# Kernel optimization log

Measured on AMD Instinct MI355X. Metric: run time of the kernel, lower is better.

Reference implementation:

```python
import jax, jax.numpy as jnp
import numpy as np

B, S, D = 2, 4096, 256
H, KD = 8, 256  # keras MHA built with key_dim=d_model -> per-head dim = 256
DFF = 1024
EPS = 1e-3  # keras LayerNormalization default epsilon
NEG = 1e9


def setup_inputs() -> dict:
    key = jax.random.key(0)
    ks = jax.random.split(key, 16)
    sd = 0.02
    return {
        "x": jax.random.normal(ks[0], (B, S, D), jnp.float32),
        "w_2": 128,
        "Wq": jax.random.normal(ks[1], (D, H, KD), jnp.float32) * sd,
        "bq": jnp.zeros((H, KD), jnp.float32),
        "Wk": jax.random.normal(ks[2], (D, H, KD), jnp.float32) * sd,
        "bk": jnp.zeros((H, KD), jnp.float32),
        "Wv": jax.random.normal(ks[3], (D, H, KD), jnp.float32) * sd,
        "bv": jnp.zeros((H, KD), jnp.float32),
        "Wo": jax.random.normal(ks[4], (H, KD, D), jnp.float32) * sd,
        "bo": jnp.zeros((D,), jnp.float32),
        "W1": jax.random.normal(ks[5], (D, DFF), jnp.float32) * sd,
        "b1": jnp.zeros((DFF,), jnp.float32),
        "W2": jax.random.normal(ks[6], (DFF, D), jnp.float32) * sd,
        "b2": jnp.zeros((D,), jnp.float32),
        "g1": jnp.ones((D,), jnp.float32),
        "be1": jnp.zeros((D,), jnp.float32),
        "g2": jnp.ones((D,), jnp.float32),
        "be2": jnp.zeros((D,), jnp.float32),
    }


def layer_norm(x, g, b):
    mu = jnp.mean(x, axis=-1, keepdims=True)
    var = jnp.mean(jnp.square(x - mu), axis=-1, keepdims=True)
    return (x - mu) * jax.lax.rsqrt(var + EPS) * g + b


def reference(x, w_2, Wq, bq, Wk, bk, Wv, bv, Wo, bo, W1, b1, W2, b2, g1, be1, g2, be2):
    # --- sliding-window self attention (dense scores + mask, as in source) ---
    q = jnp.einsum('bsd,dhk->bshk', x, Wq) + bq
    k = jnp.einsum('bsd,dhk->bshk', x, Wk) + bk
    v = jnp.einsum('bsd,dhk->bshk', x, Wv) + bv
    scores = jnp.einsum('bqhd,bkhd->bhqk', q, k) / jnp.sqrt(jnp.asarray(KD, x.dtype))
    idx = jnp.arange(S)
    mask = (jnp.abs(idx[:, None] - idx[None, :]) <= w_2)  # [S, S]
    scores = scores + (1.0 - mask.astype(x.dtype)) * (-NEG)
    attn = jax.nn.softmax(scores, axis=-1)
    ctx = jnp.einsum('bhqk,bkhd->bqhd', attn, v)
    attn_out = jnp.einsum('bqhd,hdo->bqo', ctx, Wo) + bo
    x = layer_norm(x + attn_out, g1, be1)
    # --- feed-forward ---
    h = jax.nn.relu(jnp.einsum('bsd,df->bsf', x, W1) + b1)
    ffn = jnp.einsum('bsf,fd->bsd', h, W2) + b2
    x = layer_norm(x + ffn, g2, be2)
    return x
```

## Files before the change

### kernel.cpp

```cpp
#include <hip/hip_runtime.h>
#include <hip/hip_bf16.h>

#define Bn 2
#define Sn 4096
#define Dn 256
#define Hn 8
#define KDn 256
#define DFFn 1024
#define Mn (Bn*Sn)
#define NQKVn (Hn*KDn)

typedef __attribute__((ext_vector_type(4))) float f32x4;
typedef __attribute__((ext_vector_type(8))) short bf16x8;
typedef __attribute__((ext_vector_type(4))) short short4v;

__device__ __forceinline__ short f2bf(float f) {
  unsigned u = __builtin_bit_cast(unsigned, f);
  unsigned r = u + 0x7fffu + ((u >> 16) & 1u);
  return (short)(r >> 16);
}

#define GLL16(gsrc, ldst) \
  __builtin_amdgcn_global_load_lds((const __attribute__((address_space(1))) void*)(gsrc), \
                                   (__attribute__((address_space(3))) void*)(ldst), 16, 0, 0)

#define WAITCNT4 asm volatile("s_waitcnt vmcnt(4)" ::: "memory")
#define WAITCNT2 asm volatile("s_waitcnt vmcnt(2)" ::: "memory")
#define WAITCNT0 asm volatile("s_waitcnt vmcnt(0)" ::: "memory")
#define BARRIER  do { __builtin_amdgcn_s_barrier(); asm volatile("" ::: "memory"); } while (0)

__global__ __launch_bounds__(256)
void cvt_x(const float* __restrict__ x, short* __restrict__ xb, int n) {
  int i = (blockIdx.x * 256 + threadIdx.x) * 4;
  if (i < n) {
    float4 v = *(const float4*)(x + i);
    short4v o = { f2bf(v.x), f2bf(v.y), f2bf(v.z), f2bf(v.w) };
    *(short4v*)(xb + i) = o;
  }
}

__global__ __launch_bounds__(256)
void concat_bias(const float* __restrict__ bq, const float* __restrict__ bk,
                 const float* __restrict__ bv, float* __restrict__ o) {
  int i = blockIdx.x * 256 + threadIdx.x;
  o[i] = (i < 2048) ? bq[i] : (i < 4096 ? bk[i - 2048] : bv[i - 4096]);
}

__global__ __launch_bounds__(256)
void cvt_weights(const float* __restrict__ Wq, const float* __restrict__ Wk,
                 const float* __restrict__ Wv, const float* __restrict__ Wo,
                 const float* __restrict__ W1, const float* __restrict__ W2,
                 short* __restrict__ WqT, short* __restrict__ WkT,
                 short* __restrict__ WvT, short* __restrict__ WoT,
                 short* __restrict__ W1T, short* __restrict__ W2T) {
  int t = blockIdx.x;
  const float* W; short* WT; int K, N;
  if      (t < 512)  { W = Wq; WT = WqT; K = 256;  N = 2048; }
  else if (t < 1024) { t -= 512;  W = Wk; WT = WkT; K = 256;  N = 2048; }
  else if (t < 1536) { t -= 1024; W = Wv; WT = WvT; K = 256;  N = 2048; }
  else if (t < 2048) { t -= 1536; W = Wo; WT = WoT; K = 2048; N = 256;  }
  else if (t < 2304) { t -= 2048; W = W1; WT = W1T; K = 256;  N = 1024; }
  else               { t -= 2304; W = W2; WT = W2T; K = 1024; N = 256;  }
  const int ktiles = K >> 5;
  const int k0 = (t % ktiles) * 32, n0 = (t / ktiles) * 32;
  __shared__ short tt[32][33];
  const int tx = threadIdx.x & 31, ty = threadIdx.x >> 5;
#pragma unroll
  for (int i = 0; i < 32; i += 8)
    tt[ty + i][tx] = f2bf(W[(size_t)(k0 + ty + i) * N + n0 + tx]);
  __syncthreads();
#pragma unroll
  for (int i = 0; i < 32; i += 8)
    WT[(size_t)(n0 + ty + i) * K + k0 + tx] = tt[tx][ty + i];
}

__global__ __launch_bounds__(256, 3)
void gemm_qkv(const short* __restrict__ A, const short* __restrict__ BT,
              const float* __restrict__ bias, short* __restrict__ Qo,
              short* __restrict__ Ko, short* __restrict__ Vto) {
  __shared__ __align__(16) short smem[3 * 8192];
  const int tid = threadIdx.x;
  const int lane = tid & 63;
  const int wave = tid >> 6;
  const int tn = blockIdx.x;
  const int tm = blockIdx.y;
  const int wr = (wave >> 1) * 64;
  const int wc = (wave & 1) * 64;
  const int lrow = lane & 15;
  const int lk = (lane >> 4) * 8;

  f32x4 acc[4][4];
#pragma unroll
  for (int i = 0; i < 4; ++i)
#pragma unroll
    for (int j = 0; j < 4; ++j) acc[i][j] = (f32x4){0.f, 0.f, 0.f, 0.f};

  const int row_s = tid >> 2;
  const int col_s = (tid & 3) * 8;
  const short* aB = A + (size_t)(tm * 128 + row_s) * 256 + col_s;
  const short* bB = BT + (size_t)(tn * 128 + row_s) * 256 + col_s;

  auto stage = [&](int kt, int bf) {
    const short* aP = aB + kt * 32;
    const short* bP = bB + kt * 32;
    short* AsB = smem + bf * 8192 + wave * 512;
    short* BsB = smem + bf * 8192 + 4096 + wave * 512;
    GLL16(aP, AsB);
    GLL16(aP + 64 * 256, AsB + 2048);
    GLL16(bP, BsB);
    GLL16(bP + 64 * 256, BsB + 2048);
  };

  stage(0, 0);
  stage(1, 1);
  int cur = 0;
  for (int kt = 0; kt < 8; ++kt) {
    if (kt == 7) WAITCNT0; else WAITCNT4;
    BARRIER;
    if (kt + 2 < 8) { int nb = cur + 2; if (nb >= 3) nb -= 3; stage(kt + 2, nb); }
    const short* As = smem + cur * 8192;
    const short* Bs = As + 4096;
    bf16x8 af[4], bfr[4];
#pragma unroll
    for (int i = 0; i < 4; ++i) {
      af[i]  = *(const bf16x8*)(As + (wr + i * 16 + lrow) * 32 + lk);
      bfr[i] = *(const bf16x8*)(Bs + (wc + i * 16 + lrow) * 32 + lk);
    }
#pragma unroll
    for (int i = 0; i < 4; ++i)
#pragma unroll
      for (int j = 0; j < 4; ++j)
        acc[i][j] = __builtin_amdgcn_mfma_f32_16x16x32_bf16(af[i], bfr[j], acc[i][j], 0, 0, 0);
    ++cur; if (cur == 3) cur = 0;
  }

  const int rbase = (lane >> 4) * 4;
  if (tn < 32) {
    short* C = (tn < 16) ? Qo : Ko;
    const float sc = (tn < 16) ? 1.f : 0.0625f;
    const int cb = (tn & 15) * 128;
#pragma unroll
    for (int j = 0; j < 4; ++j) {
      const int cj = wc + j * 16 + lrow;
      const float bv = bias[tn * 128 + cj];
      const int cl = cb + cj;
#pragma unroll
      for (int i = 0; i < 4; ++i) {
        const int row0 = tm * 128 + wr + i * 16 + rbase;
        f32x4 a = acc[i][j];
#pragma unroll
        for (int r = 0; r < 4; ++r)
          C[(size_t)(row0 + r) * NQKVn + cl] = f2bf((a[r] + bv) * sc);
      }
    }
  } else {
    __syncthreads();
    short* Ct = smem;
#pragma unroll
    for (int j = 0; j < 4; ++j) {
      const int colL = wc + j * 16 + lrow;
      const float bv = bias[tn * 128 + colL];
#pragma unroll
      for (int i = 0; i < 4; ++i) {
        const int rowL0 = wr + i * 16 + rbase;
        f32x4 a = acc[i][j];
        short4v o = { f2bf(a[0] + bv), f2bf(a[1] + bv), f2bf(a[2] + bv), f2bf(a[3] + bv) };
        *(short4v*)(&Ct[colL * 130 + rowL0]) = o;
      }
    }
    __syncthreads();
    const int kd_l = tid >> 1;
    const int so = (tid & 1) * 64;
    const int cl = (tn - 32) * 128 + kd_l;
    const int hh = cl >> 8;
    const int kd = cl & 255;
    const int row0 = tm * 128;
    const int bb = row0 >> 12;
    const int s0 = (row0 & (Sn - 1)) + so;
    short* dst = Vto + (size_t)((bb * Hn + hh) * KDn + kd) * Sn + s0;
#pragma unroll
    for (int u = 0; u < 64; u += 8)
      *(bf16x8*)(dst + u) = *(const bf16x8*)(&Ct[kd_l * 130 + so + u]);
  }
}

__global__ __launch_bounds__(256, 3)
void gemm_ffn1(const short* __restrict__ A, const short* __restrict__ BT,
               const float* __restrict__ bias, short* __restrict__ C,
               int N, int K) {
  __shared__ __align__(16) short smem[3 * 8192];
  const int tid = threadIdx.x;
  const int lane = tid & 63;
  const int wave = tid >> 6;
  const int tn = blockIdx.x;
  const int tm = blockIdx.y;
  const int wr = (wave >> 1) * 64;
  const int wc = (wave & 1) * 64;
  const int lrow = lane & 15;
  const int lk = (lane >> 4) * 8;

  f32x4 acc[4][4];
#pragma unroll
  for (int i = 0; i < 4; ++i)
#pragma unroll
    for (int j = 0; j < 4; ++j) acc[i][j] = (f32x4){0.f, 0.f, 0.f, 0.f};

  const int row_s = tid >> 2;
  const int col_s = (tid & 3) * 8;
  const short* aB = A + (size_t)(tm * 128 + row_s) * K + col_s;
  const short* bB = BT + (size_t)(tn * 128 + row_s) * K + col_s;

  auto stage = [&](int kt, int bf) {
    const short* aP = aB + kt * 32;
    const short* bP = bB + kt * 32;
    short* AsB = smem + bf * 8192 + wave * 512;
    short* BsB = smem + bf * 8192 + 4096 + wave * 512;
    GLL16(aP, AsB);
    GLL16(aP + (size_t)64 * K, AsB + 2048);
    GLL16(bP, BsB);
    GLL16(bP + (size_t)64 * K, BsB + 2048);
  };

  const int nk = K >> 5;
  stage(0, 0);
  if (nk > 1) stage(1, 1);
  int cur = 0;
  for (int kt = 0; kt < nk; ++kt) {
    if (kt == nk - 1) WAITCNT0; else WAITCNT4;
    BARRIER;
    if (kt + 2 < nk) { int nb = cur + 2; if (nb >= 3) nb -= 3; stage(kt + 2, nb); }
    const short* As = smem + cur * 8192;
    const short* Bs = As + 4096;
    bf16x8 af[4], bfr[4];
#pragma unroll
    for (int i = 0; i < 4; ++i) {
      af[i]  = *(const bf16x8*)(As + (wr + i * 16 + lrow) * 32 + lk);
      bfr[i] = *(const bf16x8*)(Bs + (wc + i * 16 + lrow) * 32 + lk);
    }
#pragma unroll
    for (int i = 0; i < 4; ++i)
#pragma unroll
      for (int j = 0; j < 4; ++j)
        acc[i][j] = __builtin_amdgcn_mfma_f32_16x16x32_bf16(af[i], bfr[j], acc[i][j], 0, 0, 0);
    ++cur; if (cur == 3) cur = 0;
  }

  const int rbase = (lane >> 4) * 4;
#pragma unroll
  for (int j = 0; j < 4; ++j) {
    const int col = tn * 128 + wc + j * 16 + lrow;
    const float bv = bias[col];
#pragma unroll
    for (int i = 0; i < 4; ++i) {
      const int row0 = tm * 128 + wr + i * 16 + rbase;
      f32x4 a = acc[i][j];
#pragma unroll
      for (int r = 0; r < 4; ++r)
        C[(size_t)(row0 + r) * N + col] = f2bf(fmaxf(a[r] + bv, 0.f));
    }
  }
}

__global__ __launch_bounds__(256, 4)
void gemm_bt64(const short* __restrict__ A, const short* __restrict__ BT,
               const float* __restrict__ bias, float* __restrict__ C,
               int N, int K) {
  __shared__ __align__(16) short smem[3 * 4096];
  const int tid = threadIdx.x;
  const int lane = tid & 63;
  const int wave = tid >> 6;
  const int tn = blockIdx.x;
  const int tm = blockIdx.y;
  const int wr = (wave >> 1) * 32;
  const int wc = (wave & 1) * 32;
  const int lrow = lane & 15;
  const int lk = (lane >> 4) * 8;

  f32x4 acc[2][2];
#pragma unroll
  for (int i = 0; i < 2; ++i)
#pragma unroll
    for (int j = 0; j < 2; ++j) acc[i][j] = (f32x4){0.f, 0.f, 0.f, 0.f};

  const int row_s = tid >> 2;
  const int col_s = (tid & 3) * 8;
  const short* aB = A + (size_t)(tm * 64 + row_s) * K + col_s;
  const short* bB = BT + (size_t)(tn * 64 + row_s) * K + col_s;

  auto stage = [&](int kt, int bf) {
    GLL16(aB + kt * 32, smem + bf * 4096 + wave * 512);
    GLL16(bB + kt * 32, smem + bf * 4096 + 2048 + wave * 512);
  };

  const int nk = K >> 5;
  stage(0, 0);
  if (nk > 1) stage(1, 1);
  int cur = 0;
  for (int kt = 0; kt < nk; ++kt) {
    if (kt == nk - 1) WAITCNT0; else WAITCNT2;
    BARRIER;
    if (kt + 2 < nk) { int nb = cur + 2; if (nb >= 3) nb -= 3; stage(kt + 2, nb); }
    const short* As = smem + cur * 4096;
    const short* Bs = As + 2048;
    bf16x8 af[2], bfr[2];
#pragma unroll
    for (int i = 0; i < 2; ++i) {
      af[i]  = *(const bf16x8*)(As + (wr + i * 16 + lrow) * 32 + lk);
      bfr[i] = *(const bf16x8*)(Bs + (wc + i * 16 + lrow) * 32 + lk);
    }
#pragma unroll
    for (int i = 0; i < 2; ++i)
#pragma unroll
      for (int j = 0; j < 2; ++j)
        acc[i][j] = __builtin_amdgcn_mfma_f32_16x16x32_bf16(af[i], bfr[j], acc[i][j], 0, 0, 0);
    ++cur; if (cur == 3) cur = 0;
  }

  const int rbase = (lane >> 4) * 4;
#pragma unroll
  for (int j = 0; j < 2; ++j) {
    const int col = tn * 64 + wc + j * 16 + lrow;
    const float bv = bias[col];
#pragma unroll
    for (int i = 0; i < 2; ++i) {
      const int row0 = tm * 64 + wr + i * 16 + rbase;
      f32x4 a = acc[i][j];
#pragma unroll
      for (int r = 0; r < 4; ++r) C[(size_t)(row0 + r) * N + col] = a[r] + bv;
    }
  }
}

__global__ __launch_bounds__(512, 1)
void attn_win(const short* __restrict__ q, const short* __restrict__ k,
              const short* __restrict__ vt, short* __restrict__ ctx,
              const int* __restrict__ w2p) {
  const int bid = blockIdx.x;
  const int swz = (bid & 7) * 32 + (bid >> 3);
  const int q0 = (swz & 15) * 256;
  const int h = (swz >> 4) & 7;
  const int b = swz >> 7;
  const int tid = threadIdx.x;
  const int lane = tid & 63;
  const int wave = tid >> 6;
  const int w2 = *w2p;
  const int qw = q0 + wave * 32;
  const int lrow = lane & 15;
  const int lk = (lane >> 4) * 8;
  const int lk2 = lk * 2;
  const int rbase = (lane >> 4) * 4;

  __shared__ __align__(16) short Ks[3][8192];
  __shared__ __align__(16) short Vs[3][8192];
  __shared__ __align__(16) short Ps[8][1024];
  short* P = Ps[wave];

  const short* qbase = q + (size_t)(b * Sn + qw) * NQKVn + h * KDn;
  bf16x8 qf[2][8];
#pragma unroll
  for (int mi = 0; mi < 2; ++mi)
#pragma unroll
    for (int ks = 0; ks < 8; ++ks)
      qf[mi][ks] = *(const bf16x8*)(qbase + (size_t)(mi * 16 + lrow) * NQKVn + ks * 32 + lk);

  f32x4 oacc[2][16];
#pragma unroll
  for (int mi = 0; mi < 2; ++mi)
#pragma unroll
    for (int nc = 0; nc < 16; ++nc) oacc[mi][nc] = (f32x4){0.f, 0.f, 0.f, 0.f};

  float lsum[2][4];
#pragma unroll
  for (int mi = 0; mi < 2; ++mi)
#pragma unroll
    for (int r = 0; r < 4; ++r) lsum[mi][r] = 0.f;

  const short* kbase = k + (size_t)(b * Sn) * NQKVn + h * KDn;
  const short* vtb = vt + (size_t)((b * Hn + h) * KDn) * Sn;

  int bstart = q0 - w2; if (bstart < 0) bstart = 0; bstart &= ~31;
  int bend = q0 + 256 + w2; if (bend > Sn) bend = Sn; bend = (bend + 31) & ~31;
  int wlo = qw - w2; if (wlo < 0) wlo = 0; wlo &= ~31;
  int whi = qw + 32 + w2; if (whi > Sn) whi = Sn;

  auto stage = [&](int c0, int bf) {
#pragma unroll
    for (int e = 0; e < 2; ++e) {
      const int o = e * 8192 + tid * 16;
      const int row = o >> 9;
      const int cc = (o & 511) ^ ((row & 7) << 4);
      GLL16(kbase + (size_t)(c0 + row) * NQKVn + (cc >> 1),
            (char*)Ks[bf] + e * 8192 + wave * 1024);
    }
#pragma unroll
    for (int e = 0; e < 2; ++e) {
      const int o = e * 8192 + tid * 16;
      const int row = o >> 6;
      const int cc = (o & 63) ^ ((row & 3) << 4);
      GLL16(vtb + (size_t)row * Sn + c0 + (cc >> 1),
            (char*)Vs[bf] + e * 8192 + wave * 1024);
    }
  };

  const int nch = (bend - bstart) >> 5;
  stage(bstart, 0);
  if (nch > 1) stage(bstart + 32, 1);

  int cur = 0;
  for (int i = 0; i < nch; ++i) {
    const int c0 = bstart + i * 32;
    if (i == nch - 1) WAITCNT0; else WAITCNT4;
    BARRIER;
    if (i + 2 < nch) { int nb = cur + 2; if (nb >= 3) nb -= 3; stage(c0 + 64, nb); }

    if (c0 >= wlo && c0 < whi) {
      const char* Kc = (const char*)Ks[cur];
      const int x0 = (lrow & 7) << 4;
      f32x4 sf[2][2];
      sf[0][0] = sf[0][1] = sf[1][0] = sf[1][1] = (f32x4){0.f, 0.f, 0.f, 0.f};
#pragma unroll
      for (int ks = 0; ks < 8; ++ks) {
        const int cb = (lk2 + ks * 64) ^ x0;
        bf16x8 kf0 = *(const bf16x8*)(Kc + lrow * 512 + cb);
        bf16x8 kf1 = *(const bf16x8*)(Kc + (16 + lrow) * 512 + cb);
        sf[0][0] = __builtin_amdgcn_mfma_f32_16x16x32_bf16(qf[0][ks], kf0, sf[0][0], 0, 0, 0);
        sf[0][1] = __builtin_amdgcn_mfma_f32_16x16x32_bf16(qf[0][ks], kf1, sf[0][1], 0, 0, 0);
        sf[1][0] = __builtin_amdgcn_mfma_f32_16x16x32_bf16(qf[1][ks], kf0, sf[1][0], 0, 0, 0);
        sf[1][1] = __builtin_amdgcn_mfma_f32_16x16x32_bf16(qf[1][ks], kf1, sf[1][1], 0, 0, 0);
      }
      const bool full = (c0 >= qw + 31 - w2) && (c0 + 31 <= qw + w2);
      if (full) {
#pragma unroll
        for (int mi = 0; mi < 2; ++mi)
#pragma unroll
          for (int ni = 0; ni < 2; ++ni)
#pragma unroll
            for (int r = 0; r < 4; ++r) {
              const float p = __expf(sf[mi][ni][r]);
              sf[mi][ni][r] = p;
              lsum[mi][r] += p;
            }
      } else {
#pragma unroll
        for (int mi = 0; mi < 2; ++mi)
#pragma unroll
          for (int ni = 0; ni < 2; ++ni) {
            const int kk = c0 + ni * 16 + lrow;
#pragma unroll
            for (int r = 0; r < 4; ++r) {
              const int dd = (qw + mi * 16 + rbase + r) - kk;
              const bool val = (dd <= w2) && (dd >= -w2);
              float p = __expf(sf[mi][ni][r]);
              p = val ? p : 0.f;
              sf[mi][ni][r] = p;
              lsum[mi][r] += p;
            }
          }
      }
#pragma unroll
      for (int mi = 0; mi < 2; ++mi)
#pragma unroll
        for (int ni = 0; ni < 2; ++ni)
#pragma unroll
          for (int r = 0; r < 4; ++r)
            P[(mi * 16 + rbase + r) * 32 + ni * 16 + lrow] = f2bf(sf[mi][ni][r]);

      bf16x8 pa0 = *(const bf16x8*)(P + lrow * 32 + lk);
      bf16x8 pa1 = *(const bf16x8*)(P + (16 + lrow) * 32 + lk);
      const char* Vc = (const char*)Vs[cur] + lrow * 64 + (lk2 ^ ((lrow & 3) << 4));
#pragma unroll
      for (int nc = 0; nc < 16; ++nc) {
        bf16x8 vf = *(const bf16x8*)(Vc + nc * 1024);
        oacc[0][nc] = __builtin_amdgcn_mfma_f32_16x16x32_bf16(pa0, vf, oacc[0][nc], 0, 0, 0);
        oacc[1][nc] = __builtin_amdgcn_mfma_f32_16x16x32_bf16(pa1, vf, oacc[1][nc], 0, 0, 0);
      }
    }
    ++cur; if (cur == 3) cur = 0;
  }

#pragma unroll
  for (int mi = 0; mi < 2; ++mi)
#pragma unroll
    for (int r = 0; r < 4; ++r) {
      float s = lsum[mi][r];
#pragma unroll
      for (int d = 1; d < 16; d <<= 1) s += __shfl_xor(s, d);
      lsum[mi][r] = 1.f / s;
    }

  short* cbase = ctx + (size_t)(b * Sn + qw) * NQKVn + h * KDn;
#pragma unroll
  for (int mi = 0; mi < 2; ++mi)
#pragma unroll
    for (int nc = 0; nc < 16; ++nc)
#pragma unroll
      for (int r = 0; r < 4; ++r)
        cbase[(size_t)(mi * 16 + rbase + r) * NQKVn + nc * 16 + lrow] =
            f2bf(oacc[mi][nc][r] * lsum[mi][r]);
}

__global__ __launch_bounds__(256)
void ln_fused(const float* __restrict__ xin, const float* __restrict__ yin,
              const float* __restrict__ g, const float* __restrict__ bb,
              float* __restrict__ of32, short* __restrict__ obf) {
  const int row = blockIdx.x * 4 + (threadIdx.x >> 6);
  const int lane = threadIdx.x & 63;
  const size_t base = (size_t)row * Dn + lane * 4;
  float4 a = *(const float4*)(xin + base);
  float4 bv = *(const float4*)(yin + base);
  float4 v = { a.x + bv.x, a.y + bv.y, a.z + bv.z, a.w + bv.w };
  float sum = v.x + v.y + v.z + v.w;
  float ssq = v.x * v.x + v.y * v.y + v.z * v.z + v.w * v.w;
#pragma unroll
  for (int d = 1; d < 64; d <<= 1) { sum += __shfl_xor(sum, d); ssq += __shfl_xor(ssq, d); }
  const float mu = sum * (1.f / Dn);
  const float var = ssq * (1.f / Dn) - mu * mu;
  const float rs = rsqrtf(var + 1e-3f);
  float4 gg = *(const float4*)(g + lane * 4);
  float4 bbv = *(const float4*)(bb + lane * 4);
  float4 o = { (v.x - mu) * rs * gg.x + bbv.x, (v.y - mu) * rs * gg.y + bbv.y,
               (v.z - mu) * rs * gg.z + bbv.z, (v.w - mu) * rs * gg.w + bbv.w };
  if (of32) *(float4*)(of32 + base) = o;
  if (obf) {
    short4v ob = { f2bf(o.x), f2bf(o.y), f2bf(o.z), f2bf(o.w) };
    *(short4v*)(obf + base) = ob;
  }
}

extern "C" void kernel_launch(void* const* d_in, const int* in_sizes, int n_in,
                              void* d_out, int out_size, void* d_ws, size_t ws_size,
                              hipStream_t stream) {
  const float* x   = (const float*)d_in[0];
  const int*   w2p = (const int*)d_in[1];
  const float* Wq  = (const float*)d_in[2];
  const float* bq  = (const float*)d_in[3];
  const float* Wk  = (const float*)d_in[4];
  const float* bk  = (const float*)d_in[5];
  const float* Wv  = (const float*)d_in[6];
  const float* bv  = (const float*)d_in[7];
  const float* Wo  = (const float*)d_in[8];
  const float* bo  = (const float*)d_in[9];
  const float* W1  = (const float*)d_in[10];
  const float* b1  = (const float*)d_in[11];
  const float* W2  = (const float*)d_in[12];
  const float* b2  = (const float*)d_in[13];
  const float* g1  = (const float*)d_in[14];
  const float* be1 = (const float*)d_in[15];
  const float* g2  = (const float*)d_in[16];
  const float* be2 = (const float*)d_in[17];
  float* out = (float*)d_out;

  char* ws = (char*)d_ws;
  size_t off = 0;
  auto alloc = [&](size_t bytes) { void* p = ws + off; off += (bytes + 255) & ~(size_t)255; return p; };
  short* xb    = (short*)alloc((size_t)Mn * Dn * 2);
  short* WqkvT = (short*)alloc((size_t)3 * NQKVn * Dn * 2);
  float* bqkv  = (float*)alloc((size_t)3 * NQKVn * 4);
  short* WoT   = (short*)alloc((size_t)Dn * NQKVn * 2);
  short* W1T   = (short*)alloc((size_t)DFFn * Dn * 2);
  short* W2T   = (short*)alloc((size_t)Dn * DFFn * 2);
  short* qb    = (short*)alloc((size_t)Mn * NQKVn * 2);
  short* kb    = (short*)alloc((size_t)Mn * NQKVn * 2);
  short* vtb   = (short*)alloc((size_t)Mn * NQKVn * 2);
  float* attn_out = (float*)alloc((size_t)Mn * Dn * 4);
  float* x1    = (float*)alloc((size_t)Mn * Dn * 4);
  short* ctxb = qb;
  short* x1b  = xb;
  short* hb   = kb;
  float* ffn  = attn_out;

  cvt_x<<<dim3(Mn * Dn / 1024), dim3(256), 0, stream>>>(x, xb, Mn * Dn);
  cvt_weights<<<dim3(2560), dim3(256), 0, stream>>>(
      Wq, Wk, Wv, Wo, W1, W2,
      WqkvT, WqkvT + (size_t)NQKVn * Dn, WqkvT + (size_t)2 * NQKVn * Dn,
      WoT, W1T, W2T);
  concat_bias<<<dim3(24), dim3(256), 0, stream>>>(bq, bk, bv, bqkv);

  gemm_qkv<<<dim3(48, 64), dim3(256), 0, stream>>>(xb, WqkvT, bqkv, qb, kb, vtb);

  attn_win<<<dim3(256), dim3(512), 0, stream>>>(qb, kb, vtb, ctxb, w2p);

  gemm_bt64<<<dim3(Dn / 64, Mn / 64), dim3(256), 0, stream>>>(ctxb, WoT, bo, attn_out, Dn, NQKVn);
  ln_fused<<<dim3(Mn / 4), dim3(256), 0, stream>>>(x, attn_out, g1, be1, x1, x1b);
  gemm_ffn1<<<dim3(DFFn / 128, Mn / 128), dim3(256), 0, stream>>>(x1b, W1T, b1, hb, DFFn, Dn);
  gemm_bt64<<<dim3(Dn / 64, Mn / 64), dim3(256), 0, stream>>>(hb, W2T, b2, ffn, Dn, DFFn);
  ln_fused<<<dim3(Mn / 4), dim3(256), 0, stream>>>(x1, ffn, g2, be2, out, (short*)nullptr);
}
```

Measured before the change: 187.5 us.

## Stage GEMM epilogues through LDS, add MFMA priority, use exp2 softmax, pad P

The Q/K and ReLU GEMM epilogues now write bf16 results into a padded LDS tile and then emit coalesced 16-byte row stores, replacing scattered 2-byte global stores. s_setprio is raised around the MFMA blocks in all GEMMs. The K scale folds in log2(e) so the attention kernel can use exp2f instead of __expf. The per-wave P buffer gets a row stride of 40 to reduce LDS bank conflicts. The cost is extra barriers and LDS traffic in the epilogues and slightly more shared memory in attention.

Result: slower. 201.9 us (+7.7%).

```diff
diff --git a/kernel.cpp b/kernel.cpp
--- a/kernel.cpp
+++ b/kernel.cpp
@@ -126,33 +126,43 @@
       af[i]  = *(const bf16x8*)(As + (wr + i * 16 + lrow) * 32 + lk);
       bfr[i] = *(const bf16x8*)(Bs + (wc + i * 16 + lrow) * 32 + lk);
     }
+    __builtin_amdgcn_s_setprio(1);
 #pragma unroll
     for (int i = 0; i < 4; ++i)
 #pragma unroll
       for (int j = 0; j < 4; ++j)
         acc[i][j] = __builtin_amdgcn_mfma_f32_16x16x32_bf16(af[i], bfr[j], acc[i][j], 0, 0, 0);
+    __builtin_amdgcn_s_setprio(0);
     ++cur; if (cur == 3) cur = 0;
   }
 
   const int rbase = (lane >> 4) * 4;
   if (tn < 32) {
     short* C = (tn < 16) ? Qo : Ko;
-    const float sc = (tn < 16) ? 1.f : 0.0625f;
+    const float sc = (tn < 16) ? 1.f : (0.0625f * 1.4426950408889634f);
     const int cb = (tn & 15) * 128;
+    __syncthreads();
+    short* Ct = smem;
 #pragma unroll
     for (int j = 0; j < 4; ++j) {
-      const int cj = wc + j * 16 + lrow;
-      const float bv = bias[tn * 128 + cj];
-      const int cl = cb + cj;
+      const int colL = wc + j * 16 + lrow;
+      const float bv = bias[tn * 128 + colL];
 #pragma unroll
       for (int i = 0; i < 4; ++i) {
-        const int row0 = tm * 128 + wr + i * 16 + rbase;
+        const int rowL = wr + i * 16 + rbase;
         f32x4 a = acc[i][j];
 #pragma unroll
         for (int r = 0; r < 4; ++r)
-          C[(size_t)(row0 + r) * NQKVn + cl] = f2bf((a[r] + bv) * sc);
+          Ct[(rowL + r) * 136 + colL] = f2bf((a[r] + bv) * sc);
       }
     }
+    __syncthreads();
+    const int row = tid >> 1;
+    const int seg = (tid & 1) * 64;
+    short* dst = C + (size_t)(tm * 128 + row) * NQKVn + cb + seg;
+#pragma unroll
+    for (int u = 0; u < 64; u += 8)
+      *(bf16x8*)(dst + u) = *(const bf16x8*)(&Ct[row * 136 + seg + u]);
   } else {
     __syncthreads();
     short* Ct = smem;
@@ -237,28 +247,39 @@
       af[i]  = *(const bf16x8*)(As + (wr + i * 16 + lrow) * 32 + lk);
       bfr[i] = *(const bf16x8*)(Bs + (wc + i * 16 + lrow) * 32 + lk);
     }
+    __builtin_amdgcn_s_setprio(1);
 #pragma unroll
     for (int i = 0; i < 4; ++i)
 #pragma unroll
       for (int j = 0; j < 4; ++j)
         acc[i][j] = __builtin_amdgcn_mfma_f32_16x16x32_bf16(af[i], bfr[j], acc[i][j], 0, 0, 0);
+    __builtin_amdgcn_s_setprio(0);
     ++cur; if (cur == 3) cur = 0;
   }
 
   const int rbase = (lane >> 4) * 4;
+  __syncthreads();
+  short* Ct = smem;
 #pragma unroll
   for (int j = 0; j < 4; ++j) {
-    const int col = tn * 128 + wc + j * 16 + lrow;
-    const float bv = bias[col];
+    const int colL = wc + j * 16 + lrow;
+    const float bv = bias[tn * 128 + colL];
 #pragma unroll
     for (int i = 0; i < 4; ++i) {
-      const int row0 = tm * 128 + wr + i * 16 + rbase;
+      const int rowL = wr + i * 16 + rbase;
       f32x4 a = acc[i][j];
 #pragma unroll
       for (int r = 0; r < 4; ++r)
-        C[(size_t)(row0 + r) * N + col] = f2bf(fmaxf(a[r] + bv, 0.f));
-    }
-  }
+        Ct[(rowL + r) * 136 + colL] = f2bf(fmaxf(a[r] + bv, 0.f));
+    }
+  }
+  __syncthreads();
+  const int row = tid >> 1;
+  const int seg = (tid & 1) * 64;
+  short* dst = C + (size_t)(tm * 128 + row) * N + tn * 128 + seg;
+#pragma unroll
+  for (int u = 0; u < 64; u += 8)
+    *(bf16x8*)(dst + u) = *(const bf16x8*)(&Ct[row * 136 + seg + u]);
 }
 
 __global__ __launch_bounds__(256, 4)
@@ -308,11 +329,13 @@
       af[i]  = *(const bf16x8*)(As + (wr + i * 16 + lrow) * 32 + lk);
       bfr[i] = *(const bf16x8*)(Bs + (wc + i * 16 + lrow) * 32 + lk);
     }
+    __builtin_amdgcn_s_setprio(1);
 #pragma unroll
     for (int i = 0; i < 2; ++i)
 #pragma unroll
       for (int j = 0; j < 2; ++j)
         acc[i][j] = __builtin_amdgcn_mfma_f32_16x16x32_bf16(af[i], bfr[j], acc[i][j], 0, 0, 0);
+    __builtin_amdgcn_s_setprio(0);
     ++cur; if (cur == 3) cur = 0;
   }
 
@@ -352,7 +375,7 @@
 
   __shared__ __align__(16) short Ks[3][8192];
   __shared__ __align__(16) short Vs[3][8192];
-  __shared__ __align__(16) short Ps[8][1024];
+  __shared__ __align__(16) short Ps[8][1280];
   short* P = Ps[wave];
 
   const short* qbase = q + (size_t)(b * Sn + qw) * NQKVn + h * KDn;
@@ -436,7 +459,7 @@
           for (int ni = 0; ni < 2; ++ni)
 #pragma unroll
             for (int r = 0; r < 4; ++r) {
-              const float p = __expf(sf[mi][ni][r]);
+              const float p = exp2f(sf[mi][ni][r]);
               sf[mi][ni][r] = p;
               lsum[mi][r] += p;
             }
@@ -450,7 +473,7 @@
             for (int r = 0; r < 4; ++r) {
               const int dd = (qw + mi * 16 + rbase + r) - kk;
               const bool val = (dd <= w2) && (dd >= -w2);
-              float p = __expf(sf[mi][ni][r]);
+              float p = exp2f(sf[mi][ni][r]);
               p = val ? p : 0.f;
               sf[mi][ni][r] = p;
               lsum[mi][r] += p;
@@ -463,10 +486,10 @@
         for (int ni = 0; ni < 2; ++ni)
 #pragma unroll
           for (int r = 0; r < 4; ++r)
-            P[(mi * 16 + rbase + r) * 32 + ni * 16 + lrow] = f2bf(sf[mi][ni][r]);
-
-      bf16x8 pa0 = *(const bf16x8*)(P + lrow * 32 + lk);
-      bf16x8 pa1 = *(const bf16x8*)(P + (16 + lrow) * 32 + lk);
+            P[(mi * 16 + rbase + r) * 40 + ni * 16 + lrow] = f2bf(sf[mi][ni][r]);
+
+      bf16x8 pa0 = *(const bf16x8*)(P + lrow * 40 + lk);
+      bf16x8 pa1 = *(const bf16x8*)(P + (16 + lrow) * 40 + lk);
       const char* Vc = (const char*)Vs[cur] + lrow * 64 + (lk2 ^ ((lrow & 3) << 4));
 #pragma unroll
       for (int nc = 0; nc < 16; ++nc) {
```
